# Kernel optimization log

Hardware: AMD Instinct MI355X
Metric: run time of the kernel (lower is better)

## Reference

```python
import jax, jax.numpy as jnp
import numpy as np

D_MODEL = 1024
N_HEADS = 16
K_RETRIEVED = 32
BANK_SIZE = 131072
EPS = 1e-12  # matches F.normalize eps


def setup_inputs() -> dict:
    key = jax.random.key(0)
    ks = jax.random.split(key, 7)
    B, T = 8, 2048
    x = jax.random.normal(ks[0], (B, T, D_MODEL), dtype=jnp.float32)
    mem_keys = jax.random.normal(ks[1], (BANK_SIZE, D_MODEL), dtype=jnp.float32)
    mem_values = jax.random.normal(ks[2], (BANK_SIZE, D_MODEL), dtype=jnp.float32)
    s = 1.0 / np.sqrt(D_MODEL)
    Wq = jax.random.normal(ks[3], (D_MODEL, D_MODEL), dtype=jnp.float32) * s
    Wk = jax.random.normal(ks[4], (D_MODEL, D_MODEL), dtype=jnp.float32) * s
    Wv = jax.random.normal(ks[5], (D_MODEL, D_MODEL), dtype=jnp.float32) * s
    Wo = jax.random.normal(ks[6], (D_MODEL, D_MODEL), dtype=jnp.float32) * s
    gate_logit = jnp.zeros((1,), dtype=jnp.float32)
    return {"x": x, "mem_keys": mem_keys, "mem_values": mem_values,
            "Wq": Wq, "Wk": Wk, "Wv": Wv, "Wo": Wo, "gate_logit": gate_logit}


def _normalize(v):
    n = jnp.linalg.norm(v, axis=-1, keepdims=True)
    return v / jnp.maximum(n, EPS)


def reference(x, mem_keys, mem_values, Wq, Wk, Wv, Wo, gate_logit):
    B, T, D = x.shape
    H, hd, k = N_HEADS, D_MODEL // N_HEADS, K_RETRIEVED

    # --- retrieval: mean-pool query, cosine-sim top-k, gather values ---
    q = x.mean(axis=1)                       # (B, D)
    sims = _normalize(q) @ _normalize(mem_keys).T   # (B, BANK_SIZE)
    _, idx = jax.lax.top_k(sims, k)          # (B, k) descending
    retrieved = mem_values[idx]              # (B, k, d_mem)

    # --- cross-attention over retrieved docs ---
    Q = (x @ Wq).reshape(B, T, H, hd)
    K = (retrieved @ Wk).reshape(B, k, H, hd)
    V = (retrieved @ Wv).reshape(B, k, H, hd)
    scale = 1.0 / jnp.sqrt(jnp.asarray(hd, dtype=x.dtype))
    attn = jnp.einsum('bthd,bkhd->bhtk', Q, K) * scale
    attn = jax.nn.softmax(attn, axis=-1)
    ctx = jnp.einsum('bhtk,bkhd->bthd', attn, V).reshape(B, T, D)
    ctx = ctx @ Wo

    gate = jax.nn.sigmoid(gate_logit)        # (1,) broadcasts
    return x + gate * ctx
```

## Files before the change

### kernel.cpp

```cpp
#include <hip/hip_runtime.h>

#define D_MODEL 1024
#define NH 16
#define HD 64
#define KRET 32
#define BANK 131072
#define BB 8
#define TT 2048
#define MTOK 16384
#define EPSN 1e-12f

typedef __attribute__((ext_vector_type(8))) short bf16x8;
typedef __attribute__((ext_vector_type(8))) unsigned short u16x8;
typedef __attribute__((ext_vector_type(4))) float f32x4;

__device__ __forceinline__ unsigned short f2bf(float f) {
  unsigned int u = __float_as_uint(f);
  u += 0x7fffu + ((u >> 16) & 1u);
  return (unsigned short)(u >> 16);
}
__device__ __forceinline__ float bf2f(unsigned short h) {
  return __uint_as_float(((unsigned int)h) << 16);
}

__device__ __forceinline__ void gload16(const void* g, void* l) {
  __builtin_amdgcn_global_load_lds(
      (const __attribute__((address_space(1))) unsigned int*)g,
      (__attribute__((address_space(3))) unsigned int*)l, 16, 0, 0);
}

__global__ __launch_bounds__(256) void k_conv_mean(const float* __restrict__ x,
                                                   unsigned short* __restrict__ xb,
                                                   float* __restrict__ part) {
  int ch = blockIdx.x, b = blockIdx.y, tid = threadIdx.x;
  const float4* xp = (const float4*)(x + ((size_t)b * TT + ch * 32) * D_MODEL);
  ushort4* xo = (ushort4*)(xb + ((size_t)b * TT + ch * 32) * D_MODEL);
  float4 acc = {0.f, 0.f, 0.f, 0.f};
#pragma unroll 4
  for (int t = 0; t < 32; t++) {
    float4 v = xp[t * 256 + tid];
    acc.x += v.x; acc.y += v.y; acc.z += v.z; acc.w += v.w;
    ushort4 o;
    o.x = f2bf(v.x); o.y = f2bf(v.y); o.z = f2bf(v.z); o.w = f2bf(v.w);
    xo[t * 256 + tid] = o;
  }
  ((float4*)part)[((size_t)b * 64 + ch) * 256 + tid] = acc;
}

__global__ __launch_bounds__(256) void k_transW(const float* W0, const float* W1,
                                                const float* W2, const float* W3,
                                                unsigned short* T0, unsigned short* T1,
                                                unsigned short* T2, unsigned short* T3) {
  const float* W; unsigned short* T;
  switch (blockIdx.z) {
    case 0: W = W0; T = T0; break;
    case 1: W = W1; T = T1; break;
    case 2: W = W2; T = T2; break;
    default: W = W3; T = T3; break;
  }
  __shared__ float tile[64][65];
  int k0 = blockIdx.y * 64, n0 = blockIdx.x * 64;
  int tid = threadIdx.x;
#pragma unroll
  for (int i = 0; i < 16; i++) {
    int idx = tid + i * 256; int r = idx >> 6, c = idx & 63;
    tile[r][c] = W[(size_t)(k0 + r) * D_MODEL + n0 + c];
  }
  __syncthreads();
#pragma unroll
  for (int i = 0; i < 16; i++) {
    int idx = tid + i * 256; int r = idx >> 6, c = idx & 63;
    T[(size_t)(n0 + r) * D_MODEL + k0 + c] = f2bf(tile[c][r]);
  }
}

__global__ __launch_bounds__(256) void k_qnorm(const float* __restrict__ part,
                                               float* __restrict__ qn) {
  int b = blockIdx.x; int tid = threadIdx.x;
  __shared__ float red[4];
  const float4* pp = (const float4*)part + (size_t)b * 64 * 256 + tid;
  float4 a = {0.f, 0.f, 0.f, 0.f};
#pragma unroll 8
  for (int p = 0; p < 64; p++) {
    float4 v = pp[(size_t)p * 256];
    a.x += v.x; a.y += v.y; a.z += v.z; a.w += v.w;
  }
  const float sc = 1.f / (float)TT;
  a.x *= sc; a.y *= sc; a.z *= sc; a.w *= sc;
  float ss = a.x * a.x + a.y * a.y + a.z * a.z + a.w * a.w;
#pragma unroll
  for (int m = 32; m >= 1; m >>= 1) ss += __shfl_xor(ss, m);
  if ((tid & 63) == 0) red[tid >> 6] = ss;
  __syncthreads();
  float tot = red[0] + red[1] + red[2] + red[3];
  float inv = 1.f / fmaxf(sqrtf(tot), EPSN);
  float4 o = {a.x * inv, a.y * inv, a.z * inv, a.w * inv};
  ((float4*)qn)[(size_t)b * 256 + tid] = o;
}

__global__ __launch_bounds__(256) void k_sims(const float* __restrict__ mk,
                                              const float* __restrict__ qn,
                                              float* __restrict__ sims) {
  int wave = threadIdx.x >> 6, lane = threadIdx.x & 63;
  int row0 = (blockIdx.x * 4 + wave) * 4;
  float4 kv[4][4];
#pragma unroll
  for (int r = 0; r < 4; r++) {
    const float4* kr = (const float4*)(mk + (size_t)(row0 + r) * D_MODEL);
#pragma unroll
    for (int i = 0; i < 4; i++) kv[r][i] = kr[lane + 64 * i];
  }
  float ss[4] = {0.f, 0.f, 0.f, 0.f};
#pragma unroll
  for (int r = 0; r < 4; r++)
#pragma unroll
    for (int i = 0; i < 4; i++)
      ss[r] += kv[r][i].x * kv[r][i].x + kv[r][i].y * kv[r][i].y +
               kv[r][i].z * kv[r][i].z + kv[r][i].w * kv[r][i].w;
  float dots[8][4];
#pragma unroll
  for (int b = 0; b < 8; b++)
#pragma unroll
    for (int r = 0; r < 4; r++) dots[b][r] = 0.f;
#pragma unroll
  for (int b = 0; b < 8; b++) {
    const float4* qb = (const float4*)(qn + (size_t)b * D_MODEL);
#pragma unroll
    for (int i = 0; i < 4; i++) {
      float4 q4 = qb[lane + 64 * i];
#pragma unroll
      for (int r = 0; r < 4; r++)
        dots[b][r] += kv[r][i].x * q4.x + kv[r][i].y * q4.y +
                      kv[r][i].z * q4.z + kv[r][i].w * q4.w;
    }
  }
#pragma unroll
  for (int m = 32; m >= 1; m >>= 1) {
#pragma unroll
    for (int r = 0; r < 4; r++) ss[r] += __shfl_xor(ss[r], m);
#pragma unroll
    for (int b = 0; b < 8; b++)
#pragma unroll
      for (int r = 0; r < 4; r++) dots[b][r] += __shfl_xor(dots[b][r], m);
  }
  if (lane == 0) {
#pragma unroll
    for (int r = 0; r < 4; r++) {
      float inv = 1.f / fmaxf(sqrtf(ss[r]), EPSN);
#pragma unroll
      for (int b = 0; b < 8; b++)
        sims[(size_t)b * BANK + row0 + r] = dots[b][r] * inv;
    }
  }
}

__global__ __launch_bounds__(256) void k_topk_local(const float* __restrict__ sims,
                                                    float* __restrict__ cval,
                                                    int* __restrict__ cidx) {
  int b = blockIdx.y, chunk = blockIdx.x;
  int tid = threadIdx.x, wave = tid >> 6, lane = tid & 63;
  const float* sb = sims + (size_t)b * BANK + chunk * 2048;
  float v[8]; int gi[8];
#pragma unroll
  for (int j = 0; j < 8; j++) {
    int loc = j * 256 + tid;
    v[j] = sb[loc];
    gi[j] = chunk * 2048 + loc;
  }
  __shared__ float wv[4]; __shared__ int wi[4];
  __shared__ int bcast;
  for (int it = 0; it < KRET; ++it) {
    float best = -1e30f; int besti = 1 << 30;
#pragma unroll
    for (int j = 0; j < 8; j++)
      if (v[j] > best || (v[j] == best && gi[j] < besti)) { best = v[j]; besti = gi[j]; }
#pragma unroll
    for (int m = 32; m >= 1; m >>= 1) {
      float ov = __shfl_xor(best, m); int oi = __shfl_xor(besti, m);
      if (ov > best || (ov == best && oi < besti)) { best = ov; besti = oi; }
    }
    if (lane == 0) { wv[wave] = best; wi[wave] = besti; }
    __syncthreads();
    if (tid == 0) {
      float fb = wv[0]; int fi = wi[0];
      for (int w = 1; w < 4; w++)
        if (wv[w] > fb || (wv[w] == fb && wi[w] < fi)) { fb = wv[w]; fi = wi[w]; }
      bcast = fi;
      cval[((size_t)b * 64 + chunk) * KRET + it] = fb;
      cidx[((size_t)b * 64 + chunk) * KRET + it] = fi;
    }
    __syncthreads();
    int w = bcast;
#pragma unroll
    for (int j = 0; j < 8; j++)
      if (gi[j] == w) v[j] = -1e30f;
  }
}

__global__ __launch_bounds__(256) void k_topk_merge(const float* __restrict__ cval,
                                                    const int* __restrict__ cidx,
                                                    int* __restrict__ idx) {
  int b = blockIdx.x;
  int tid = threadIdx.x, wave = tid >> 6, lane = tid & 63;
  const float* cv = cval + (size_t)b * 2048;
  const int* ci = cidx + (size_t)b * 2048;
  float v[8]; int gi[8];
#pragma unroll
  for (int j = 0; j < 8; j++) {
    int loc = j * 256 + tid;
    v[j] = cv[loc];
    gi[j] = ci[loc];
  }
  __shared__ float wv[4]; __shared__ int wi[4];
  __shared__ int bcast;
  for (int it = 0; it < KRET; ++it) {
    float best = -1e30f; int besti = 1 << 30;
#pragma unroll
    for (int j = 0; j < 8; j++)
      if (v[j] > best || (v[j] == best && gi[j] < besti)) { best = v[j]; besti = gi[j]; }
#pragma unroll
    for (int m = 32; m >= 1; m >>= 1) {
      float ov = __shfl_xor(best, m); int oi = __shfl_xor(besti, m);
      if (ov > best || (ov == best && oi < besti)) { best = ov; besti = oi; }
    }
    if (lane == 0) { wv[wave] = best; wi[wave] = besti; }
    __syncthreads();
    if (tid == 0) {
      float fb = wv[0]; int fi = wi[0];
      for (int w = 1; w < 4; w++)
        if (wv[w] > fb || (wv[w] == fb && wi[w] < fi)) { fb = wv[w]; fi = wi[w]; }
      bcast = fi;
      idx[b * KRET + it] = fi;
    }
    __syncthreads();
    int w = bcast;
#pragma unroll
    for (int j = 0; j < 8; j++)
      if (gi[j] == w) v[j] = -1e30f;
  }
}

__global__ __launch_bounds__(256) void k_kvgemm(const float* __restrict__ mv,
                                                const int* __restrict__ idx_g,
                                                const unsigned short* __restrict__ Bt,
                                                float* __restrict__ Kout,
                                                float* __restrict__ Vout) {
  __shared__ __align__(16) unsigned short As[128 * 32];
  __shared__ __align__(16) unsigned short Bs[128 * 32];
  __shared__ int idxs[128];
  const int tid = threadIdx.x;
  const int wave = tid >> 6, lane = tid & 63;
  const int bm = blockIdx.x * 128, bn = blockIdx.y * 128;
  const int wm = (wave >> 1) * 64, wn = (wave & 1) * 64;
  const int frow = lane & 15, kg = lane >> 4;
  const int K = 1024;

  if (tid < 128) idxs[tid] = idx_g[bm + tid];
  __syncthreads();

  f32x4 acc[4][4] = {};

  const int row0 = tid >> 2, col0 = (tid & 3) * 8;
  const int row1 = row0 + 64;
  const int g0 = tid * 8;
  const int g1 = 2048 + tid * 8;
  const unsigned short* b0 = Bt + (size_t)(bn + (g0 >> 5)) * K + (g0 & 31);
  const unsigned short* b1 = Bt + (size_t)(bn + (g1 >> 5)) * K + (g1 & 31);
  unsigned short* lB0 = &Bs[wave * 512];
  unsigned short* lB1 = &Bs[2048 + wave * 512];
  const float* src0 = mv + (size_t)idxs[row0] * D_MODEL + col0;
  const float* src1 = mv + (size_t)idxs[row1] * D_MODEL + col0;

  for (int k0 = 0; k0 < K; k0 += 32) {
    gload16(b0 + k0, lB0);
    gload16(b1 + k0, lB1);
    float4 u0 = *(const float4*)(src0 + k0);
    float4 w0 = *(const float4*)(src0 + k0 + 4);
    float4 u1 = *(const float4*)(src1 + k0);
    float4 w1 = *(const float4*)(src1 + k0 + 4);
    u16x8 p0, p1;
    p0[0] = f2bf(u0.x); p0[1] = f2bf(u0.y); p0[2] = f2bf(u0.z); p0[3] = f2bf(u0.w);
    p0[4] = f2bf(w0.x); p0[5] = f2bf(w0.y); p0[6] = f2bf(w0.z); p0[7] = f2bf(w0.w);
    p1[0] = f2bf(u1.x); p1[1] = f2bf(u1.y); p1[2] = f2bf(u1.z); p1[3] = f2bf(u1.w);
    p1[4] = f2bf(w1.x); p1[5] = f2bf(w1.y); p1[6] = f2bf(w1.z); p1[7] = f2bf(w1.w);
    *(u16x8*)&As[row0 * 32 + col0] = p0;
    *(u16x8*)&As[row1 * 32 + col0] = p1;
    __syncthreads();
    bf16x8 fa[4], fb[4];
#pragma unroll
    for (int i = 0; i < 4; i++)
      fa[i] = *(const bf16x8*)&As[(wm + i * 16 + frow) * 32 + kg * 8];
#pragma unroll
    for (int i = 0; i < 4; i++)
      fb[i] = *(const bf16x8*)&Bs[(wn + i * 16 + frow) * 32 + kg * 8];
#pragma unroll
    for (int i = 0; i < 4; i++)
#pragma unroll
      for (int j = 0; j < 4; j++)
        acc[i][j] = __builtin_amdgcn_mfma_f32_16x16x32_bf16(fa[i], fb[j], acc[i][j], 0, 0, 0);
    __syncthreads();
  }

  const int crow = (lane >> 4) * 4, ccol = lane & 15;
#pragma unroll
  for (int i = 0; i < 4; i++)
#pragma unroll
    for (int j = 0; j < 4; j++)
#pragma unroll
      for (int r = 0; r < 4; r++) {
        int gm = bm + wm + i * 16 + crow + r;
        int gn = bn + wn + j * 16 + ccol;
        int b = gm >> 5, jj = gm & 31;
        if (gn < 1024) {
          int h = gn >> 6, d = gn & 63;
          Kout[((((size_t)b * NH + h) * KRET + jj) << 6) + d] = acc[i][j][r];
        } else {
          int gn2 = gn - 1024;
          int h = gn2 >> 6, d = gn2 & 63;
          Vout[((((size_t)b * NH + h) * KRET + jj) << 6) + d] = acc[i][j][r];
        }
      }
}

template <int MODE>
__global__ __launch_bounds__(256) void k_gemm(const unsigned short* __restrict__ A,
                                              const unsigned short* __restrict__ Bt,
                                              float* __restrict__ out_f,
                                              unsigned short* __restrict__ out_b,
                                              const float* __restrict__ xres,
                                              const float* __restrict__ gatep) {
  __shared__ __align__(16) unsigned short As[128 * 32];
  __shared__ __align__(16) unsigned short Bs[128 * 32];
  const int tid = threadIdx.x;
  const int wave = tid >> 6, lane = tid & 63;
  const int bm = blockIdx.x * 128, bn = blockIdx.y * 128;
  const int wm = (wave >> 1) * 64, wn = (wave & 1) * 64;
  const int frow = lane & 15, kg = lane >> 4;
  const int K = 1024;

  f32x4 acc[4][4] = {};

  const int g0 = tid * 8;
  const int g1 = 2048 + tid * 8;
  const unsigned short* a0 = A + (size_t)(bm + (g0 >> 5)) * K + (g0 & 31);
  const unsigned short* a1 = A + (size_t)(bm + (g1 >> 5)) * K + (g1 & 31);
  const unsigned short* b0 = Bt + (size_t)(bn + (g0 >> 5)) * K + (g0 & 31);
  const unsigned short* b1 = Bt + (size_t)(bn + (g1 >> 5)) * K + (g1 & 31);
  unsigned short* lA0 = &As[wave * 512];
  unsigned short* lA1 = &As[2048 + wave * 512];
  unsigned short* lB0 = &Bs[wave * 512];
  unsigned short* lB1 = &Bs[2048 + wave * 512];

  for (int k0 = 0; k0 < K; k0 += 32) {
    gload16(a0 + k0, lA0);
    gload16(a1 + k0, lA1);
    gload16(b0 + k0, lB0);
    gload16(b1 + k0, lB1);
    __syncthreads();
    bf16x8 fa[4], fb[4];
#pragma unroll
    for (int i = 0; i < 4; i++)
      fa[i] = *(const bf16x8*)&As[(wm + i * 16 + frow) * 32 + kg * 8];
#pragma unroll
    for (int i = 0; i < 4; i++)
      fb[i] = *(const bf16x8*)&Bs[(wn + i * 16 + frow) * 32 + kg * 8];
#pragma unroll
    for (int i = 0; i < 4; i++)
#pragma unroll
      for (int j = 0; j < 4; j++)
        acc[i][j] = __builtin_amdgcn_mfma_f32_16x16x32_bf16(fa[i], fb[j], acc[i][j], 0, 0, 0);
    __syncthreads();
  }

  const int crow = (lane >> 4) * 4, ccol = lane & 15;
  if (MODE == 2) {
    float gate = 1.f / (1.f + __expf(-gatep[0]));
#pragma unroll
    for (int i = 0; i < 4; i++)
#pragma unroll
      for (int j = 0; j < 4; j++)
#pragma unroll
        for (int r = 0; r < 4; r++) {
          int gm = bm + wm + i * 16 + crow + r;
          int gn = bn + wn + j * 16 + ccol;
          size_t off = (size_t)gm * D_MODEL + gn;
          out_f[off] = xres[off] + gate * acc[i][j][r];
        }
  } else {
#pragma unroll
    for (int i = 0; i < 4; i++)
#pragma unroll
      for (int j = 0; j < 4; j++)
#pragma unroll
        for (int r = 0; r < 4; r++) {
          int gm = bm + wm + i * 16 + crow + r;
          int gn = bn + wn + j * 16 + ccol;
          int b = gm >> 11, t = gm & 2047, h = gn >> 6, d = gn & 63;
          out_b[((((size_t)b * NH + h) * TT + t) << 6) + d] = f2bf(acc[i][j][r]);
        }
  }
}

__global__ __launch_bounds__(256) void k_attn(const unsigned short* __restrict__ Qb,
                                              const float* __restrict__ Kws,
                                              const float* __restrict__ Vws,
                                              unsigned short* __restrict__ ctx) {
  __shared__ __align__(16) float Ks[KRET * HD];
  __shared__ __align__(16) float Vs[KRET * HD];
  int bh = blockIdx.y; int b = bh >> 4, h = bh & 15;
  int tid = threadIdx.x;
  int t = blockIdx.x * 256 + tid;
  const float4* kp = (const float4*)(Kws + (size_t)bh * KRET * HD);
  const float4* vp = (const float4*)(Vws + (size_t)bh * KRET * HD);
  ((float4*)Ks)[tid] = kp[tid];
  ((float4*)Ks)[tid + 256] = kp[tid + 256];
  ((float4*)Vs)[tid] = vp[tid];
  ((float4*)Vs)[tid + 256] = vp[tid + 256];
  __syncthreads();

  const uint4* qp = (const uint4*)(Qb + ((size_t)bh * TT + t) * HD);
  float q[64];
#pragma unroll
  for (int i = 0; i < 8; i++) {
    uint4 u = qp[i];
    unsigned vals[4] = {u.x, u.y, u.z, u.w};
#pragma unroll
    for (int w = 0; w < 4; w++) {
      q[i * 8 + w * 2 + 0] = bf2f((unsigned short)(vals[w] & 0xffffu));
      q[i * 8 + w * 2 + 1] = bf2f((unsigned short)(vals[w] >> 16));
    }
  }
  float s[KRET];
#pragma unroll
  for (int j = 0; j < KRET; j++) {
    const float4* kr = (const float4*)&Ks[j * HD];
    float a = 0.f;
#pragma unroll
    for (int d4 = 0; d4 < 16; d4++) {
      float4 kk = kr[d4];
      a += q[d4 * 4 + 0] * kk.x + q[d4 * 4 + 1] * kk.y +
           q[d4 * 4 + 2] * kk.z + q[d4 * 4 + 3] * kk.w;
    }
    s[j] = a * 0.125f;
  }
  float m = s[0];
#pragma unroll
  for (int j = 1; j < KRET; j++) m = fmaxf(m, s[j]);
  float sum = 0.f;
#pragma unroll
  for (int j = 0; j < KRET; j++) { s[j] = __expf(s[j] - m); sum += s[j]; }
  float inv = 1.f / sum;
  float o[64];
#pragma unroll
  for (int d = 0; d < 64; d++) o[d] = 0.f;
#pragma unroll
  for (int j = 0; j < KRET; j++) {
    float p = s[j] * inv;
    const float4* vr = (const float4*)&Vs[j * HD];
#pragma unroll
    for (int d4 = 0; d4 < 16; d4++) {
      float4 vv = vr[d4];
      o[d4 * 4 + 0] += p * vv.x; o[d4 * 4 + 1] += p * vv.y;
      o[d4 * 4 + 2] += p * vv.z; o[d4 * 4 + 3] += p * vv.w;
    }
  }
  unsigned short* cp = ctx + ((size_t)(b * TT + t)) * D_MODEL + h * HD;
#pragma unroll
  for (int d4 = 0; d4 < 16; d4++) {
    ushort4 w4;
    w4.x = f2bf(o[d4 * 4 + 0]); w4.y = f2bf(o[d4 * 4 + 1]);
    w4.z = f2bf(o[d4 * 4 + 2]); w4.w = f2bf(o[d4 * 4 + 3]);
    ((ushort4*)cp)[d4] = w4;
  }
}

extern "C" void kernel_launch(void* const* d_in, const int* in_sizes, int n_in,
                              void* d_out, int out_size, void* d_ws, size_t ws_size,
                              hipStream_t stream) {
  const float* x = (const float*)d_in[0];
  const float* mk = (const float*)d_in[1];
  const float* mv = (const float*)d_in[2];
  const float* Wq = (const float*)d_in[3];
  const float* Wk = (const float*)d_in[4];
  const float* Wv = (const float*)d_in[5];
  const float* Wo = (const float*)d_in[6];
  const float* gatep = (const float*)d_in[7];
  float* out = (float*)d_out;

  char* ws = (char*)d_ws;
  unsigned short* xb   = (unsigned short*)(ws);
  unsigned short* Qb   = (unsigned short*)(ws + 33554432);
  unsigned short* WqT  = (unsigned short*)(ws + 67108864);
  unsigned short* WkvT = (unsigned short*)(ws + 69206016);
  unsigned short* WoT  = (unsigned short*)(ws + 73400320);
  float* qn    = (float*)(ws + 75497472);
  float* sims  = (float*)(ws + 75530240);
  float* part  = (float*)(ws + 75530240);
  int*   idx   = (int*)(ws + 79724544);
  float* cval  = (float*)(ws + 79725568);
  int*   cidxb = (int*)(ws + 79791104);
  float* Kws   = (float*)(ws + 79856640);
  float* Vws   = (float*)(ws + 80905216);

  k_conv_mean<<<dim3(64, 8), 256, 0, stream>>>(x, xb, part);
  k_transW<<<dim3(16, 16, 4), 256, 0, stream>>>(Wq, Wk, Wv, Wo,
                                                WqT, WkvT, WkvT + 1048576, WoT);
  k_qnorm<<<dim3(8), 256, 0, stream>>>(part, qn);
  k_sims<<<dim3(BANK / 16), 256, 0, stream>>>(mk, qn, sims);
  k_topk_local<<<dim3(64, 8), 256, 0, stream>>>(sims, cval, cidxb);
  k_topk_merge<<<dim3(8), 256, 0, stream>>>(cval, cidxb, idx);
  k_kvgemm<<<dim3(2, 16), 256, 0, stream>>>(mv, idx, WkvT, Kws, Vws);
  k_gemm<0><<<dim3(128, 8), 256, 0, stream>>>(xb, WqT, nullptr, Qb, nullptr, nullptr);
  k_attn<<<dim3(8, 128), 256, 0, stream>>>(Qb, Kws, Vws, xb);
  k_gemm<2><<<dim3(128, 8), 256, 0, stream>>>(xb, WoT, out, nullptr, x, gatep);
}
```

Measured before the change: 505.3 us.

## Use bf16 MFMA for retrieval cross-attention scores and context

Rewrites the small-k attention kernel so QK^T and P·V run on 16x16x32 bf16 MFMA instructions rather than per-thread scalar FMAs over 64-element register arrays. K and V are converted to bf16 in shared memory, with V transposed. Softmax probabilities are staged per wave through LDS to re-layout them as an MFMA A operand. This cuts ALU work and register pressure, but adds bf16 rounding of K, V and P, plus scattered 2-byte global stores for ctx.

```diff
diff --git a/kernel.cpp b/kernel.cpp
--- a/kernel.cpp
+++ b/kernel.cpp
@@ -405,72 +405,92 @@
                                               const float* __restrict__ Kws,
                                               const float* __restrict__ Vws,
                                               unsigned short* __restrict__ ctx) {
-  __shared__ __align__(16) float Ks[KRET * HD];
-  __shared__ __align__(16) float Vs[KRET * HD];
-  int bh = blockIdx.y; int b = bh >> 4, h = bh & 15;
-  int tid = threadIdx.x;
-  int t = blockIdx.x * 256 + tid;
-  const float4* kp = (const float4*)(Kws + (size_t)bh * KRET * HD);
-  const float4* vp = (const float4*)(Vws + (size_t)bh * KRET * HD);
-  ((float4*)Ks)[tid] = kp[tid];
-  ((float4*)Ks)[tid + 256] = kp[tid + 256];
-  ((float4*)Vs)[tid] = vp[tid];
-  ((float4*)Vs)[tid + 256] = vp[tid + 256];
+  __shared__ __align__(16) unsigned short Kl[32 * 72];
+  __shared__ __align__(16) unsigned short Vt[64 * 40];
+  __shared__ __align__(16) unsigned short Pl[4][16 * 40];
+  const int bh = blockIdx.y, b = bh >> 4, h = bh & 15;
+  const int tid = threadIdx.x, wave = tid >> 6, lane = tid & 63;
+  const int t0b = blockIdx.x * 256;
+  {
+    int doc = tid >> 3, d0 = (tid & 7) * 8;
+    const float4* kp = (const float4*)(Kws + ((size_t)bh * KRET + doc) * HD + d0);
+    float4 k0 = kp[0], k1 = kp[1];
+    u16x8 kb;
+    kb[0] = f2bf(k0.x); kb[1] = f2bf(k0.y); kb[2] = f2bf(k0.z); kb[3] = f2bf(k0.w);
+    kb[4] = f2bf(k1.x); kb[5] = f2bf(k1.y); kb[6] = f2bf(k1.z); kb[7] = f2bf(k1.w);
+    *(u16x8*)&Kl[doc * 72 + d0] = kb;
+    const float4* vp = (const float4*)(Vws + ((size_t)bh * KRET + doc) * HD + d0);
+    float4 v0 = vp[0], v1 = vp[1];
+    float vv[8] = {v0.x, v0.y, v0.z, v0.w, v1.x, v1.y, v1.z, v1.w};
+#pragma unroll
+    for (int j = 0; j < 8; j++) Vt[(d0 + j) * 40 + doc] = f2bf(vv[j]);
+  }
   __syncthreads();
 
-  const uint4* qp = (const uint4*)(Qb + ((size_t)bh * TT + t) * HD);
-  float q[64];
-#pragma unroll
-  for (int i = 0; i < 8; i++) {
-    uint4 u = qp[i];
-    unsigned vals[4] = {u.x, u.y, u.z, u.w};
-#pragma unroll
-    for (int w = 0; w < 4; w++) {
-      q[i * 8 + w * 2 + 0] = bf2f((unsigned short)(vals[w] & 0xffffu));
-      q[i * 8 + w * 2 + 1] = bf2f((unsigned short)(vals[w] >> 16));
-    }
-  }
-  float s[KRET];
-#pragma unroll
-  for (int j = 0; j < KRET; j++) {
-    const float4* kr = (const float4*)&Ks[j * HD];
-    float a = 0.f;
-#pragma unroll
-    for (int d4 = 0; d4 < 16; d4++) {
-      float4 kk = kr[d4];
-      a += q[d4 * 4 + 0] * kk.x + q[d4 * 4 + 1] * kk.y +
-           q[d4 * 4 + 2] * kk.z + q[d4 * 4 + 3] * kk.w;
-    }
-    s[j] = a * 0.125f;
-  }
-  float m = s[0];
-#pragma unroll
-  for (int j = 1; j < KRET; j++) m = fmaxf(m, s[j]);
-  float sum = 0.f;
-#pragma unroll
-  for (int j = 0; j < KRET; j++) { s[j] = __expf(s[j] - m); sum += s[j]; }
-  float inv = 1.f / sum;
-  float o[64];
-#pragma unroll
-  for (int d = 0; d < 64; d++) o[d] = 0.f;
-#pragma unroll
-  for (int j = 0; j < KRET; j++) {
-    float p = s[j] * inv;
-    const float4* vr = (const float4*)&Vs[j * HD];
-#pragma unroll
-    for (int d4 = 0; d4 < 16; d4++) {
-      float4 vv = vr[d4];
-      o[d4 * 4 + 0] += p * vv.x; o[d4 * 4 + 1] += p * vv.y;
-      o[d4 * 4 + 2] += p * vv.z; o[d4 * 4 + 3] += p * vv.w;
-    }
-  }
-  unsigned short* cp = ctx + ((size_t)(b * TT + t)) * D_MODEL + h * HD;
-#pragma unroll
-  for (int d4 = 0; d4 < 16; d4++) {
-    ushort4 w4;
-    w4.x = f2bf(o[d4 * 4 + 0]); w4.y = f2bf(o[d4 * 4 + 1]);
-    w4.z = f2bf(o[d4 * 4 + 2]); w4.w = f2bf(o[d4 * 4 + 3]);
-    ((ushort4*)cp)[d4] = w4;
+  const int fr = lane & 15, kg = lane >> 4;
+  const bf16x8 kb00 = *(const bf16x8*)&Kl[fr * 72 + kg * 8];
+  const bf16x8 kb01 = *(const bf16x8*)&Kl[fr * 72 + 32 + kg * 8];
+  const bf16x8 kb10 = *(const bf16x8*)&Kl[(16 + fr) * 72 + kg * 8];
+  const bf16x8 kb11 = *(const bf16x8*)&Kl[(16 + fr) * 72 + 32 + kg * 8];
+  bf16x8 vbf[4];
+#pragma unroll
+  for (int dt = 0; dt < 4; dt++)
+    vbf[dt] = *(const bf16x8*)&Vt[(dt * 16 + fr) * 40 + kg * 8];
+  unsigned short* pw = &Pl[wave][0];
+
+#pragma unroll
+  for (int sub = 0; sub < 4; ++sub) {
+    const int t0 = t0b + wave * 64 + sub * 16;
+    const unsigned short* qrow = Qb + ((size_t)bh * TT + t0 + fr) * HD + kg * 8;
+    bf16x8 qa0 = *(const bf16x8*)(qrow);
+    bf16x8 qa1 = *(const bf16x8*)(qrow + 32);
+    f32x4 s0 = {}, s1 = {};
+    s0 = __builtin_amdgcn_mfma_f32_16x16x32_bf16(qa0, kb00, s0, 0, 0, 0);
+    s0 = __builtin_amdgcn_mfma_f32_16x16x32_bf16(qa1, kb01, s0, 0, 0, 0);
+    s1 = __builtin_amdgcn_mfma_f32_16x16x32_bf16(qa0, kb10, s1, 0, 0, 0);
+    s1 = __builtin_amdgcn_mfma_f32_16x16x32_bf16(qa1, kb11, s1, 0, 0, 0);
+    float a0[4], a1[4], mr[4], e0[4], e1[4], sr[4];
+#pragma unroll
+    for (int r = 0; r < 4; r++) {
+      a0[r] = s0[r] * 0.125f; a1[r] = s1[r] * 0.125f;
+      mr[r] = fmaxf(a0[r], a1[r]);
+    }
+#pragma unroll
+    for (int m = 1; m < 16; m <<= 1)
+#pragma unroll
+      for (int r = 0; r < 4; r++) mr[r] = fmaxf(mr[r], __shfl_xor(mr[r], m));
+#pragma unroll
+    for (int r = 0; r < 4; r++) {
+      e0[r] = __expf(a0[r] - mr[r]); e1[r] = __expf(a1[r] - mr[r]);
+      sr[r] = e0[r] + e1[r];
+    }
+#pragma unroll
+    for (int m = 1; m < 16; m <<= 1)
+#pragma unroll
+      for (int r = 0; r < 4; r++) sr[r] += __shfl_xor(sr[r], m);
+#pragma unroll
+    for (int r = 0; r < 4; r++) {
+      float inv = 1.f / sr[r];
+      int tl = (lane >> 4) * 4 + r;
+      pw[tl * 40 + fr] = f2bf(e0[r] * inv);
+      pw[tl * 40 + 16 + fr] = f2bf(e1[r] * inv);
+    }
+    asm volatile("s_waitcnt lgkmcnt(0)" ::: "memory");
+    bf16x8 pa = *(const bf16x8*)&pw[fr * 40 + kg * 8];
+    f32x4 c[4];
+#pragma unroll
+    for (int dt = 0; dt < 4; dt++) {
+      f32x4 z = {};
+      c[dt] = __builtin_amdgcn_mfma_f32_16x16x32_bf16(pa, vbf[dt], z, 0, 0, 0);
+    }
+#pragma unroll
+    for (int r = 0; r < 4; r++) {
+      int tl = (lane >> 4) * 4 + r;
+      unsigned short* crow = ctx + ((size_t)(b * TT + t0 + tl)) * D_MODEL + h * HD;
+#pragma unroll
+      for (int dt = 0; dt < 4; dt++)
+        crow[dt * 16 + fr] = f2bf(c[dt][r]);
+    }
   }
 }
 
```

After: 466.4 us. 1.08x faster.
